# Performance work log

Hardware: AMD Instinct MI355X
Metric: run time of the kernel (lower is better)

## Reference

```python
import jax, jax.numpy as jnp
import numpy as np
from jax import lax

T, B, D, H = 2048, 64, 256, 256


def setup_inputs() -> dict:
    key = jax.random.key(0)
    ks = jax.random.split(key, 9)
    s_in = 1.0 / np.sqrt(D + H)  # torch nn.Linear default init range
    inp = {
        "inputs": jax.random.normal(ks[0], (T, B, D), dtype=jnp.float32),
        "Wf": jax.random.uniform(ks[1], (D + H, H), jnp.float32, -s_in, s_in),
        "bf": jax.random.uniform(ks[2], (H,), jnp.float32, -s_in, s_in),
        "Wi": jax.random.uniform(ks[3], (D + H, H), jnp.float32, -s_in, s_in),
        "bi": jax.random.uniform(ks[4], (H,), jnp.float32, -s_in, s_in),
        "Wg": jax.random.uniform(ks[5], (D + H, H), jnp.float32, -s_in, s_in),
        "bg": jax.random.uniform(ks[6], (H,), jnp.float32, -s_in, s_in),
        "Wo": jax.random.uniform(ks[7], (D + H, H), jnp.float32, -s_in, s_in),
        "bo": jax.random.uniform(ks[8], (H,), jnp.float32, -s_in, s_in),
    }
    return inp


def reference(inputs, Wf, bf, Wi, bi, Wg, bg, Wo, bo):
    # inputs: [T, B, D] (batch_first=False), zero initial states, dropout=0.
    h0 = jnp.zeros((B, H), dtype=inputs.dtype)
    c0 = jnp.zeros((B, H), dtype=inputs.dtype)

    def step(carry, x):
        hx, cx = carry
        comb = jnp.concatenate([x, hx], axis=1)          # [B, D+H]
        f = jax.nn.sigmoid(comb @ Wf + bf)
        i = jax.nn.sigmoid(comb @ Wi + bi)
        g = jnp.tanh(comb @ Wg + bg)
        o = jax.nn.sigmoid(comb @ Wo + bo)
        cx = f * cx + i * g
        hx = o * jnp.tanh(cx)
        return (hx, cx), hx

    (hx, cx), outputs = lax.scan(step, (h0, c0), inputs)  # outputs: [T, B, H]
    return outputs, (hx, cx)
```

## Files before the change

kernel.cpp:

```cpp
#include <hip/hip_runtime.h>


typedef __attribute__((ext_vector_type(8))) short short8;
typedef __attribute__((ext_vector_type(4))) float float4v;
typedef __attribute__((ext_vector_type(4))) unsigned int uint4v;

#define TT   2048
#define BB   64
#define HH   256
#define TBH  ((size_t)33554432)
#define BH   ((size_t)16384)

#define WS_WT    0u
#define WS_BVEC  1048576u
#define WS_HBUF  1052672u
#define WS_CST   1183744u
#define WS_G     1249280u

__device__ inline unsigned short f2bf(float x) {
    unsigned u = __float_as_uint(x);
    unsigned r = (u + 0x7FFFu + ((u >> 16) & 1u)) >> 16;
    return (unsigned short)r;
}
__device__ inline float sigmoidf_(float x) { return 1.0f / (1.0f + __expf(-x)); }
__device__ inline float tanhf_(float x) {
    float e = __expf(-2.0f * fabsf(x));
    float t = (1.0f - e) / (1.0f + e);
    return copysignf(t, x);
}

__device__ inline void bar_lds() {
    asm volatile("s_waitcnt lgkmcnt(0)\n\ts_barrier" ::: "memory");
}

__global__ void k_prep_w(const float* __restrict__ Wf, const float* __restrict__ Wi,
                         const float* __restrict__ Wg, const float* __restrict__ Wo,
                         const float* __restrict__ bf_, const float* __restrict__ bi_,
                         const float* __restrict__ bg_, const float* __restrict__ bo_,
                         unsigned short* __restrict__ WT, float* __restrict__ bvec)
{
    int c = blockIdx.x;
    int gate = c >> 8, j = c & 255;
    const float* W  = (gate == 0) ? Wf : (gate == 1) ? Wi : (gate == 2) ? Wg : Wo;
    const float* bb = (gate == 0) ? bf_ : (gate == 1) ? bi_ : (gate == 2) ? bg_ : bo_;
    for (int k = threadIdx.x; k < 512; k += 256)
        WT[(size_t)c * 512 + k] = f2bf(W[(size_t)k * 256 + j]);
    if (threadIdx.x == 0) bvec[c] = bb[j];
}

__global__ void k_zero(unsigned int* __restrict__ hbuf, float* __restrict__ cst)
{
    int tid = blockIdx.x * blockDim.x + threadIdx.x;
    int nt = gridDim.x * blockDim.x;
    for (int i = tid; i < 32768; i += nt) hbuf[i] = 0u;
    for (int i = tid; i < 16384; i += nt) cst[i] = 0.f;
}

__global__ __launch_bounds__(256) void gemm_xw(
    const float* __restrict__ X,
    const unsigned short* __restrict__ WT,
    const float* __restrict__ bvec,
    float* __restrict__ G)
{
    int col0 = blockIdx.x * 128;
    int row0 = blockIdx.y * 128;
    int tid = threadIdx.x, l = tid & 63, w = tid >> 6;
    int wr = w >> 1, wc = w & 1;

    __shared__ __align__(16) unsigned char asm_[16384];
    __shared__ __align__(16) unsigned char bsm_[16384];

    float4v acc[4][4];
#pragma unroll
    for (int i = 0; i < 4; ++i)
#pragma unroll
        for (int j = 0; j < 4; ++j) { acc[i][j][0] = 0.f; acc[i][j][1] = 0.f; acc[i][j][2] = 0.f; acc[i][j][3] = 0.f; }

    for (int kt = 0; kt < 4; ++kt) {
        {
            int r = tid >> 1, seg = tid & 1;
            const float* src = X + (size_t)(row0 + r) * 256 + kt * 64 + seg * 32;
            short8 tmp[4];
#pragma unroll
            for (int v = 0; v < 4; ++v)
#pragma unroll
                for (int e = 0; e < 8; ++e) tmp[v][e] = (short)f2bf(src[v * 8 + e]);
            unsigned char* dst = asm_ + r * 128;
            int base = seg * 64, swz = (r & 7) << 4;
#pragma unroll
            for (int v = 0; v < 4; ++v)
                *(short8*)(dst + ((base + 16 * v) ^ swz)) = tmp[v];
        }
        {
            int c_ = tid >> 1, seg = tid & 1;
            const unsigned char* src = (const unsigned char*)WT + (size_t)(col0 + c_) * 1024 + kt * 128 + seg * 64;
            unsigned char* dst = bsm_ + c_ * 128;
            int base = seg * 64, swz = (c_ & 7) << 4;
#pragma unroll
            for (int v = 0; v < 4; ++v)
                *(short8*)(dst + ((base + 16 * v) ^ swz)) = *(const short8*)(src + 16 * v);
        }
        __syncthreads();
#pragma unroll
        for (int km = 0; km < 2; ++km) {
            short8 af[4], bfr[4];
            int kb = 16 * (l >> 4) + 64 * km, swz = (l & 7) << 4;
#pragma unroll
            for (int i = 0; i < 4; ++i)
                af[i] = *(const short8*)(asm_ + (wr * 64 + i * 16 + (l & 15)) * 128 + (kb ^ swz));
#pragma unroll
            for (int j = 0; j < 4; ++j)
                bfr[j] = *(const short8*)(bsm_ + (wc * 64 + j * 16 + (l & 15)) * 128 + (kb ^ swz));
#pragma unroll
            for (int i = 0; i < 4; ++i)
#pragma unroll
                for (int j = 0; j < 4; ++j)
                    acc[i][j] = __builtin_amdgcn_mfma_f32_16x16x32_bf16(af[i], bfr[j], acc[i][j], 0, 0, 0);
        }
        __syncthreads();
    }
#pragma unroll
    for (int j = 0; j < 4; ++j) {
        int col = col0 + wc * 64 + j * 16 + (l & 15);
        float bias = bvec[col];
#pragma unroll
        for (int i = 0; i < 4; ++i) {
            int row = row0 + wr * 64 + i * 16 + (l >> 4) * 4;
            float* Gp = G + (size_t)row * 1024 + col;
            Gp[0]    = acc[i][j][0] + bias;
            Gp[1024] = acc[i][j][1] + bias;
            Gp[2048] = acc[i][j][2] + bias;
            Gp[3072] = acc[i][j][3] + bias;
        }
    }
}

__global__ __launch_bounds__(512) void lstm_rec(
    const float* __restrict__ G,
    const unsigned short* __restrict__ WT,
    float* __restrict__ out,
    unsigned int* __restrict__ hbuf,
    float* __restrict__ cstate,
    int t0, int Tc)
{
    int wg = blockIdx.x;
    int g = wg & 7;
    if (g >= 4) return;
    int s = wg >> 3;

    int tid = threadIdx.x, l = tid & 63, w = tid >> 6;
    int gate = w & 3, dh = w >> 2;
    int c_lane = gate * 256 + s * 32 + dh * 16 + (l & 15);

    __shared__ __align__(16) unsigned char hsm[8192];
    __shared__ float gbuf[4][16][32];

    short8 bw[8];
    {
        const unsigned char* wp_ = (const unsigned char*)WT + (size_t)c_lane * 1024 + 512 + 16 * (l >> 4);
#pragma unroll
        for (int kk = 0; kk < 8; ++kk) bw[kk] = *(const short8*)(wp_ + 64 * kk);
    }

    int b_ = tid >> 5, j_ = tid & 31;
    float creg = cstate[(size_t)(g * 16 + b_) * 256 + s * 32 + j_];

    int srow = tid >> 5, sblk = tid & 31;
    unsigned char* hsm_dst = hsm + srow * 512 + ((sblk * 16) ^ ((srow & 7) << 4));

    for (int tl = 0; tl < Tc; ++tl) {
        int tg = t0 + tl;
        int par = tg & 1, rpar = par ^ 1;

        float4v acc;
        {
            const float* Gp = G + (size_t)(tl * 64 + g * 16) * 1024 + c_lane;
            int r0 = (l >> 4) * 4;
            acc[0] = Gp[(size_t)(r0 + 0) * 1024];
            acc[1] = Gp[(size_t)(r0 + 1) * 1024];
            acc[2] = Gp[(size_t)(r0 + 2) * 1024];
            acc[3] = Gp[(size_t)(r0 + 3) * 1024];
        }
        {
            const unsigned int* wp = hbuf + ((size_t)((g * 2 + rpar) * 16) + srow) * 256 + sblk * 8;
            unsigned want = (unsigned)tg;
            short8 hv;
            uint4v w0, w1;
            for (;;) {
                asm volatile("global_load_dwordx4 %0, %2, off sc1\n\t"
                             "global_load_dwordx4 %1, %3, off sc1\n\t"
                             "s_waitcnt vmcnt(0)"
                             : "=&v"(w0), "=&v"(w1)
                             : "v"(wp), "v"(wp + 4) : "memory");
                __builtin_amdgcn_sched_barrier(0);
                if (((w0[0] >> 16) == want) & ((w0[1] >> 16) == want) &
                    ((w0[2] >> 16) == want) & ((w0[3] >> 16) == want) &
                    ((w1[0] >> 16) == want) & ((w1[1] >> 16) == want) &
                    ((w1[2] >> 16) == want) & ((w1[3] >> 16) == want)) break;
            }
            hv[0] = (short)(w0[0] & 0xffffu);
            hv[1] = (short)(w0[1] & 0xffffu);
            hv[2] = (short)(w0[2] & 0xffffu);
            hv[3] = (short)(w0[3] & 0xffffu);
            hv[4] = (short)(w1[0] & 0xffffu);
            hv[5] = (short)(w1[1] & 0xffffu);
            hv[6] = (short)(w1[2] & 0xffffu);
            hv[7] = (short)(w1[3] & 0xffffu);
            *(short8*)hsm_dst = hv;
        }
        bar_lds();
        {
            int row = l & 15;
            const unsigned char* ap = hsm + row * 512;
            int kb0 = 16 * (l >> 4), swz = (row & 7) << 4;
            short8 af[8];
#pragma unroll
            for (int kk = 0; kk < 8; ++kk) af[kk] = *(const short8*)(ap + ((kb0 + 64 * kk) ^ swz));
            float4v acc1 = {0.f, 0.f, 0.f, 0.f};
#pragma unroll
            for (int kk = 0; kk < 4; ++kk) {
                acc  = __builtin_amdgcn_mfma_f32_16x16x32_bf16(af[kk],     bw[kk],     acc,  0, 0, 0);
                acc1 = __builtin_amdgcn_mfma_f32_16x16x32_bf16(af[kk + 4], bw[kk + 4], acc1, 0, 0, 0);
            }
            acc[0] += acc1[0]; acc[1] += acc1[1]; acc[2] += acc1[2]; acc[3] += acc1[3];
        }
        {
            int r0 = (l >> 4) * 4, cc = dh * 16 + (l & 15);
            gbuf[gate][r0 + 0][cc] = acc[0];
            gbuf[gate][r0 + 1][cc] = acc[1];
            gbuf[gate][r0 + 2][cc] = acc[2];
            gbuf[gate][r0 + 3][cc] = acc[3];
        }
        bar_lds();
        {
            float f  = sigmoidf_(gbuf[0][b_][j_]);
            float i  = sigmoidf_(gbuf[1][b_][j_]);
            float gg = tanhf_(gbuf[2][b_][j_]);
            float o  = sigmoidf_(gbuf[3][b_][j_]);
            creg = f * creg + i * gg;
            float h = o * tanhf_(creg);
            unsigned word = ((unsigned)(tg + 1) << 16) | (unsigned)f2bf(h);
            __hip_atomic_store(hbuf + ((size_t)((g * 2 + par) * 16) + b_) * 256 + s * 32 + j_,
                               word, __ATOMIC_RELAXED, __HIP_MEMORY_SCOPE_AGENT);
            size_t orow = (size_t)tg * 64 + g * 16 + b_;
            out[orow * 256 + s * 32 + j_] = h;
            if (tg == TT - 1) {
                out[TBH + (size_t)(g * 16 + b_) * 256 + s * 32 + j_] = h;
                out[TBH + BH + (size_t)(g * 16 + b_) * 256 + s * 32 + j_] = creg;
            }
        }
        bar_lds();
    }
    cstate[(size_t)(g * 16 + b_) * 256 + s * 32 + j_] = creg;
}

extern "C" void kernel_launch(void* const* d_in, const int* in_sizes, int n_in,
                              void* d_out, int out_size, void* d_ws, size_t ws_size,
                              hipStream_t stream)
{
    (void)in_sizes; (void)n_in; (void)out_size;
    const float* X   = (const float*)d_in[0];
    const float* Wf  = (const float*)d_in[1];
    const float* bf_ = (const float*)d_in[2];
    const float* Wi  = (const float*)d_in[3];
    const float* bi_ = (const float*)d_in[4];
    const float* Wg  = (const float*)d_in[5];
    const float* bg_ = (const float*)d_in[6];
    const float* Wo  = (const float*)d_in[7];
    const float* bo_ = (const float*)d_in[8];
    float* out = (float*)d_out;
    unsigned char* ws = (unsigned char*)d_ws;

    unsigned short* WT   = (unsigned short*)(ws + WS_WT);
    float*          bvec = (float*)(ws + WS_BVEC);
    unsigned int*   hbuf = (unsigned int*)(ws + WS_HBUF);
    float*          cst  = (float*)(ws + WS_CST);
    float*          G    = (float*)(ws + WS_G);

    size_t avail = ws_size > WS_G ? ws_size - WS_G : 0;
    int Tc = 8;
    const int cands[7] = {512, 256, 128, 64, 32, 16, 8};
    for (int i = 0; i < 7; ++i) {
        if ((size_t)cands[i] * 64 * 1024 * 4 <= avail) { Tc = cands[i]; break; }
    }

    k_prep_w<<<1024, 256, 0, stream>>>(Wf, Wi, Wg, Wo, bf_, bi_, bg_, bo_, WT, bvec);
    k_zero<<<64, 256, 0, stream>>>(hbuf, cst);

    for (int t0 = 0; t0 < TT; t0 += Tc) {
        int R = Tc * 64;
        gemm_xw<<<dim3(8, R / 128), 256, 0, stream>>>(X + (size_t)t0 * 64 * 256, WT, bvec, G);
        lstm_rec<<<64, 512, 0, stream>>>(G, WT, out, hbuf, cst, t0, Tc);
    }
}
```

Before: 3.236 ms.

## Store precomputed input gates as bf16 in interleaved 4-row layout

The input-projection GEMM now writes its gate pre-activations as bf16 instead of fp32. It packs the 4 consecutive batch rows of each column into one 8-byte vector. The recurrent kernel then fetches its per-step gate contribution with a single vector load instead of four strided scalar loads. That load is issued before the h-polling spin and converted after it, so its latency can overlap the wait. Halving the buffer also lets the chunk size Tc double for a given workspace, meaning fewer launches. The cost is bf16 rounding of the input-gate pre-activations, which adds numerical error.

Result: no change. 3.214 ms (-0.7%).

```diff
diff --git a/kernel.cpp b/kernel.cpp
--- a/kernel.cpp
+++ b/kernel.cpp
@@ -4,6 +4,7 @@
 typedef __attribute__((ext_vector_type(8))) short short8;
 typedef __attribute__((ext_vector_type(4))) float float4v;
 typedef __attribute__((ext_vector_type(4))) unsigned int uint4v;
+typedef __attribute__((ext_vector_type(4))) unsigned short ushort4v;
 
 #define TT   2048
 #define BB   64
@@ -21,6 +22,9 @@
     unsigned u = __float_as_uint(x);
     unsigned r = (u + 0x7FFFu + ((u >> 16) & 1u)) >> 16;
     return (unsigned short)r;
+}
+__device__ inline float bf2f(unsigned short x) {
+    return __uint_as_float((unsigned)x << 16);
 }
 __device__ inline float sigmoidf_(float x) { return 1.0f / (1.0f + __expf(-x)); }
 __device__ inline float tanhf_(float x) {
@@ -60,7 +64,7 @@
     const float* __restrict__ X,
     const unsigned short* __restrict__ WT,
     const float* __restrict__ bvec,
-    float* __restrict__ G)
+    unsigned short* __restrict__ G2)
 {
     int col0 = blockIdx.x * 128;
     int row0 = blockIdx.y * 128;
@@ -126,17 +130,18 @@
 #pragma unroll
         for (int i = 0; i < 4; ++i) {
             int row = row0 + wr * 64 + i * 16 + (l >> 4) * 4;
-            float* Gp = G + (size_t)row * 1024 + col;
-            Gp[0]    = acc[i][j][0] + bias;
-            Gp[1024] = acc[i][j][1] + bias;
-            Gp[2048] = acc[i][j][2] + bias;
-            Gp[3072] = acc[i][j][3] + bias;
+            ushort4v v;
+            v[0] = f2bf(acc[i][j][0] + bias);
+            v[1] = f2bf(acc[i][j][1] + bias);
+            v[2] = f2bf(acc[i][j][2] + bias);
+            v[3] = f2bf(acc[i][j][3] + bias);
+            *(ushort4v*)(G2 + ((size_t)(row >> 2) * 1024 + col) * 4) = v;
         }
     }
 }
 
 __global__ __launch_bounds__(512) void lstm_rec(
-    const float* __restrict__ G,
+    const unsigned short* __restrict__ G2,
     const unsigned short* __restrict__ WT,
     float* __restrict__ out,
     unsigned int* __restrict__ hbuf,
@@ -172,14 +177,11 @@
         int tg = t0 + tl;
         int par = tg & 1, rpar = par ^ 1;
 
-        float4v acc;
-        {
-            const float* Gp = G + (size_t)(tl * 64 + g * 16) * 1024 + c_lane;
-            int r0 = (l >> 4) * 4;
-            acc[0] = Gp[(size_t)(r0 + 0) * 1024];
-            acc[1] = Gp[(size_t)(r0 + 1) * 1024];
-            acc[2] = Gp[(size_t)(r0 + 2) * 1024];
-            acc[3] = Gp[(size_t)(r0 + 3) * 1024];
+        ushort4v gv;
+        {
+            const unsigned short* Gp = G2 +
+                (((size_t)((tl * 64 + g * 16) >> 2) + (l >> 4)) * 1024 + c_lane) * 4;
+            gv = *(const ushort4v*)Gp;
         }
         {
             const unsigned int* wp = hbuf + ((size_t)((g * 2 + rpar) * 16) + srow) * 256 + sblk * 8;
@@ -208,6 +210,12 @@
             hv[7] = (short)(w1[3] & 0xffffu);
             *(short8*)hsm_dst = hv;
         }
+        asm volatile("" : "+v"(gv));
+        float4v acc;
+        acc[0] = bf2f(gv[0]);
+        acc[1] = bf2f(gv[1]);
+        acc[2] = bf2f(gv[2]);
+        acc[3] = bf2f(gv[3]);
         bar_lds();
         {
             int row = l & 15;
@@ -275,13 +283,13 @@
     float*          bvec = (float*)(ws + WS_BVEC);
     unsigned int*   hbuf = (unsigned int*)(ws + WS_HBUF);
     float*          cst  = (float*)(ws + WS_CST);
-    float*          G    = (float*)(ws + WS_G);
+    unsigned short* G2   = (unsigned short*)(ws + WS_G);
 
     size_t avail = ws_size > WS_G ? ws_size - WS_G : 0;
     int Tc = 8;
     const int cands[7] = {512, 256, 128, 64, 32, 16, 8};
     for (int i = 0; i < 7; ++i) {
-        if ((size_t)cands[i] * 64 * 1024 * 4 <= avail) { Tc = cands[i]; break; }
+        if ((size_t)cands[i] * 64 * 1024 * 2 <= avail) { Tc = cands[i]; break; }
     }
 
     k_prep_w<<<1024, 256, 0, stream>>>(Wf, Wi, Wg, Wo, bf_, bi_, bg_, bo_, WT, bvec);
@@ -289,7 +297,7 @@
 
     for (int t0 = 0; t0 < TT; t0 += Tc) {
         int R = Tc * 64;
-        gemm_xw<<<dim3(8, R / 128), 256, 0, stream>>>(X + (size_t)t0 * 64 * 256, WT, bvec, G);
-        lstm_rec<<<64, 512, 0, stream>>>(G, WT, out, hbuf, cst, t0, Tc);
-    }
-}
+        gemm_xw<<<dim3(8, R / 128), 256, 0, stream>>>(X + (size_t)t0 * 64 * 256, WT, bvec, G2);
+        lstm_rec<<<64, 512, 0, stream>>>(G2, WT, out, hbuf, cst, t0, Tc);
+    }
+}
```
